# Kernel tuning notes

Hardware: AMD Instinct MI355X
Metric: run time of the kernel (lower is better)

The kernel has to match this reference:

```python
import jax, jax.numpy as jnp
import numpy as np

B, C, H, W = 8, 256, 64, 64
R = 8
CP = max(C // R, 3)  # C' = 32


def setup_inputs() -> dict:
    key = jax.random.key(0)
    ks = jax.random.split(key, 9)
    s_in = 1.0 / np.sqrt(C)
    s_cp = 1.0 / np.sqrt(CP)
    return {
        "x": jax.random.normal(ks[0], (B, C, H, W), dtype=jnp.float32),
        "Wq": jax.random.uniform(ks[1], (CP, C), minval=-s_in, maxval=s_in, dtype=jnp.float32),
        "bq": jax.random.uniform(ks[2], (CP,), minval=-s_in, maxval=s_in, dtype=jnp.float32),
        "Wk": jax.random.uniform(ks[3], (CP, C), minval=-s_in, maxval=s_in, dtype=jnp.float32),
        "bk": jax.random.uniform(ks[4], (CP,), minval=-s_in, maxval=s_in, dtype=jnp.float32),
        "Wv": jax.random.uniform(ks[5], (CP, C), minval=-s_in, maxval=s_in, dtype=jnp.float32),
        "bv": jax.random.uniform(ks[6], (CP,), minval=-s_in, maxval=s_in, dtype=jnp.float32),
        "Wb": jax.random.uniform(ks[7], (C, CP), minval=-s_cp, maxval=s_cp, dtype=jnp.float32),
        "bb": jax.random.uniform(ks[8], (C,), minval=-s_cp, maxval=s_cp, dtype=jnp.float32),
    }


def reference(x, Wq, bq, Wk, bk, Wv, bv, Wb, bb):
    b, c, h, w = x.shape
    n = h * w
    xf = x.reshape(b, c, n)  # [B, C, N]
    # 1x1 convs == channel-wise linear projections
    q = jnp.einsum('oc,bcn->bon', Wq, xf) + bq[None, :, None]  # [B, C', N]
    k = jnp.einsum('oc,bcn->bon', Wk, xf) + bk[None, :, None]
    v = jnp.einsum('oc,bcn->bon', Wv, xf) + bv[None, :, None]
    # attention: softmax(Q^T K) over last dim -> [B, N, N]
    attn = jax.nn.softmax(jnp.einsum('bon,bom->bnm', q, k), axis=-1)
    # out[b,c,i] = sum_j v[b,c,j] * attn[b,j,i]
    out = jnp.einsum('bcj,bji->bci', v, attn)  # [B, C', N]
    back = jnp.einsum('co,bon->bcn', Wb, out) + bb[None, :, None]  # [B, C, N]
    return back.reshape(b, c, h, w) + x
```

## Files before the change

kernel.cpp:

```cpp
#include <hip/hip_runtime.h>
#include <hip/hip_bf16.h>

#define NB 8
#define CC 256
#define CP 32
#define NN 4096
#define LOG2E 1.44269504088896340736f

typedef __attribute__((ext_vector_type(8))) short short8;
typedef __attribute__((ext_vector_type(4))) float floatx4;
typedef __attribute__((ext_vector_type(4))) int intx4;

static __device__ __forceinline__ ushort bf16r(float f) {
    __hip_bfloat16 h = __float2bfloat16(f);
    return *reinterpret_cast<ushort*>(&h);
}
static __device__ __forceinline__ float bf2f(ushort u) {
    union { unsigned int i; float f; } x;
    x.i = ((unsigned int)u) << 16;
    return x.f;
}
static __device__ __forceinline__ short8 load_frag(const ushort* p) {
    intx4 v = *reinterpret_cast<const intx4*>(p);
    return *reinterpret_cast<short8*>(&v);
}
static __device__ __forceinline__ unsigned int pk2(float a, float b) {
    unsigned int ua = __float_as_uint(a) + 0x8000u;
    unsigned int ub = __float_as_uint(b) + 0x8000u;
    return (ua >> 16) | (ub & 0xFFFF0000u);
}
static __device__ __forceinline__ ushort pk1(float a) {
    return (ushort)((__float_as_uint(a) + 0x8000u) >> 16);
}
static __device__ __forceinline__ float fexp2(float x) {
#if defined(__has_builtin)
#if __has_builtin(__builtin_amdgcn_exp2f)
    return __builtin_amdgcn_exp2f(x);
#else
    return __expf(x * 0.69314718055994530942f);
#endif
#else
    return __expf(x * 0.69314718055994530942f);
#endif
}

__global__ void prep_w(const float* __restrict__ Wq, const float* __restrict__ Wk,
                       const float* __restrict__ Wv, const float* __restrict__ Wb,
                       ushort* __restrict__ W96, ushort* __restrict__ W2b) {
    int r = blockIdx.x, c = threadIdx.x;
    if (r < 96) {
        const float* src = (r < 32) ? (Wq + r * CC) : ((r < 64) ? (Wk + (r - 32) * CC) : (Wv + (r - 64) * CC));
        float scale = (r < 32) ? LOG2E : 1.0f;
        W96[r * CC + c] = bf16r(src[c] * scale);
    } else {
        int idx = (r - 96) * 256 + c;
        W2b[idx] = bf16r(Wb[idx]);
    }
}

__global__ __launch_bounds__(256) void proj_kernel(
    const float* __restrict__ x, const ushort* __restrict__ W96,
    const float* __restrict__ bq, const float* __restrict__ bk, const float* __restrict__ bv,
    ushort* __restrict__ Qt, ushort* __restrict__ Kt, ushort* __restrict__ Vt) {
    __shared__ ushort xt[64 * 264];
    int b = blockIdx.x >> 6, nt = blockIdx.x & 63;
    int t = threadIdx.x;
    int n0 = nt * 64;
    {
        int cq = t >> 4, n4 = (t & 15) * 4;
#pragma unroll
        for (int cc = 0; cc < 4; cc++) {
            int c_base = cc * 64 + cq * 4;
            float4 xv[4];
#pragma unroll
            for (int e = 0; e < 4; e++)
                xv[e] = *reinterpret_cast<const float4*>(&x[((size_t)b * CC + c_base + e) * NN + n0 + n4]);
            const float* xs = reinterpret_cast<const float*>(xv);
#pragma unroll
            for (int jj = 0; jj < 4; jj++) {
                ushort4 u;
                u.x = pk1(xs[0 * 4 + jj]);
                u.y = pk1(xs[1 * 4 + jj]);
                u.z = pk1(xs[2 * 4 + jj]);
                u.w = pk1(xs[3 * 4 + jj]);
                *reinterpret_cast<ushort4*>(&xt[(n4 + jj) * 264 + c_base]) = u;
            }
        }
    }
    __syncthreads();
    int w = t >> 6, lane = t & 63, l15 = lane & 15, q = lane >> 4;
    floatx4 acc[6];
#pragma unroll
    for (int k = 0; k < 6; k++) acc[k] = (floatx4){0.f, 0.f, 0.f, 0.f};
#pragma unroll
    for (int ks = 0; ks < 8; ks++) {
        short8 bfrag = load_frag(&xt[(w * 16 + l15) * 264 + ks * 32 + q * 8]);
#pragma unroll
        for (int ot = 0; ot < 6; ot++) {
            short8 afrag = load_frag(&W96[(size_t)(ot * 16 + l15) * CC + ks * 32 + q * 8]);
            acc[ot] = __builtin_amdgcn_mfma_f32_16x16x32_bf16(afrag, bfrag, acc[ot], 0, 0, 0);
        }
    }
    int n = n0 + w * 16 + l15;
#pragma unroll
    for (int ot = 0; ot < 6; ot++) {
        const float* bias = (ot < 2) ? bq : ((ot < 4) ? bk : bv);
        ushort* dst = (ot < 2) ? Qt : ((ot < 4) ? Kt : Vt);
        int o0 = (ot & 1) * 16 + q * 4;
        float4 b4 = *reinterpret_cast<const float4*>(bias + o0);
        float sc = (ot < 2) ? LOG2E : 1.0f;
        ushort4 pk;
        pk.x = bf16r(acc[ot][0] + b4.x * sc);
        pk.y = bf16r(acc[ot][1] + b4.y * sc);
        pk.z = bf16r(acc[ot][2] + b4.z * sc);
        pk.w = bf16r(acc[ot][3] + b4.w * sc);
        *reinterpret_cast<ushort4*>(&dst[((size_t)b * NN + n) * CP + o0]) = pk;
    }
}

__global__ __launch_bounds__(256, 4) void passA_kernel(
    const ushort* __restrict__ Qt, const ushort* __restrict__ Kt, float* __restrict__ Fp) {
    __shared__ ushort kst[256 * 40];
    int bid = blockIdx.x;
    int mq = bid & 3, jt = (bid >> 2) & 63, b = bid >> 8;
    int w = threadIdx.x >> 6, lane = threadIdx.x & 63;
    int l15 = lane & 15, q = lane >> 4;
    int j = jt * 64 + w * 16 + l15;

    short8 af = load_frag(&Qt[((size_t)b * NN + j) * CP + q * 8]);
    floatx4 lacc = (floatx4){0.f, 0.f, 0.f, 0.f};

    for (int mc = 0; mc < 4; mc++) {
        int m0 = mq * 1024 + mc * 256;
        __syncthreads();
        {
            const intx4* src = reinterpret_cast<const intx4*>(&Kt[((size_t)b * NN + m0) * CP]);
            intx4* dst = reinterpret_cast<intx4*>(kst);
#pragma unroll
            for (int s = 0; s < 4; s++) {
                int g = threadIdx.x + 256 * s;
                dst[(g >> 2) * 5 + (g & 3)] = src[g];
            }
        }
        __syncthreads();
#pragma unroll
        for (int ms = 0; ms < 16; ms++) {
            short8 bf = load_frag(&kst[(ms * 16 + l15) * 40 + q * 8]);
            floatx4 z = (floatx4){0.f, 0.f, 0.f, 0.f};
            floatx4 s = __builtin_amdgcn_mfma_f32_16x16x32_bf16(af, bf, z, 0, 0, 0);
            lacc[0] += fexp2(s[0]);
            lacc[1] += fexp2(s[1]);
            lacc[2] += fexp2(s[2]);
            lacc[3] += fexp2(s[3]);
        }
    }
#pragma unroll
    for (int d = 1; d < 16; d <<= 1) {
        lacc[0] += __shfl_xor(lacc[0], d, 64);
        lacc[1] += __shfl_xor(lacc[1], d, 64);
        lacc[2] += __shfl_xor(lacc[2], d, 64);
        lacc[3] += __shfl_xor(lacc[3], d, 64);
    }
    if (l15 == 0) {
        float4 f4;
        f4.x = lacc[0]; f4.y = lacc[1]; f4.z = lacc[2]; f4.w = lacc[3];
        *reinterpret_cast<float4*>(&Fp[((size_t)mq * NB + b) * NN + jt * 64 + w * 16 + q * 4]) = f4;
    }
}

__global__ __launch_bounds__(256) void fold_kernel(
    const ushort* __restrict__ Vt, const float* __restrict__ Fp, ushort* __restrict__ Vp) {
    __shared__ ushort tile[32 * 136];
    const size_t PL = (size_t)NB * NN;
    int b = blockIdx.x >> 5, nc = blockIdx.x & 31;
    int t = threadIdx.x;
    int half = t >> 7, nl = t & 127;
    int n = nc * 128 + nl;
    size_t bn = (size_t)b * NN + n;
    float f = 1.0f / (Fp[bn] + Fp[PL + bn] + Fp[2 * PL + bn] + Fp[3 * PL + bn]);
    const ushort* src = &Vt[bn * CP + half * 16];
#pragma unroll
    for (int g = 0; g < 2; g++) {
        intx4 raw = *reinterpret_cast<const intx4*>(src + g * 8);
        const ushort* us = reinterpret_cast<const ushort*>(&raw);
#pragma unroll
        for (int e = 0; e < 8; e++) {
            tile[(half * 16 + g * 8 + e) * 136 + nl] = pk1(bf2f(us[e]) * f);
        }
    }
    __syncthreads();
#pragma unroll
    for (int cc = 0; cc < 16; cc++) {
        int c = half * 16 + cc;
        Vp[((size_t)b * CP + c) * NN + nc * 128 + nl] = tile[c * 136 + nl];
    }
}

__global__ __launch_bounds__(256, 4) void passB_kernel(
    const ushort* __restrict__ Qt, const ushort* __restrict__ Kt, const ushort* __restrict__ Vp,
    const ushort* __restrict__ W2b, const float* __restrict__ bb, const float* __restrict__ x,
    float* __restrict__ out) {
    __shared__ ushort qst[256 * 40];
    __shared__ ushort vst[32 * 264];

    int bid = blockIdx.x;
    int it = bid & 127, b = bid >> 7;
    int w = threadIdx.x >> 6, lane = threadIdx.x & 63;
    int l15 = lane & 15, q = lane >> 4;
    int jp = w;
    int i0 = it * 32;

    short8 kf0 = load_frag(&Kt[((size_t)b * NN + i0 + l15) * CP + q * 8]);
    short8 kf1 = load_frag(&Kt[((size_t)b * NN + i0 + 16 + l15) * CP + q * 8]);

    floatx4 acc00 = (floatx4){0.f, 0.f, 0.f, 0.f};
    floatx4 acc10 = (floatx4){0.f, 0.f, 0.f, 0.f};
    floatx4 acc01 = (floatx4){0.f, 0.f, 0.f, 0.f};
    floatx4 acc11 = (floatx4){0.f, 0.f, 0.f, 0.f};

    int qrow = (l15 >> 2) * 8 + (l15 & 3);

    for (int jc = 0; jc < 16; jc++) {
        int j0 = jc * 256;
        __syncthreads();
        {
            const intx4* qsrc = reinterpret_cast<const intx4*>(&Qt[((size_t)b * NN + j0) * CP]);
            intx4* qdst = reinterpret_cast<intx4*>(qst);
#pragma unroll
            for (int s = 0; s < 4; s++) {
                int g = threadIdx.x + 256 * s;
                qdst[(g >> 2) * 5 + (g & 3)] = qsrc[g];
            }
            int r = threadIdx.x >> 3, ci = threadIdx.x & 7;
            const intx4* vsrc = reinterpret_cast<const intx4*>(&Vp[((size_t)b * CP + r) * NN + j0]);
            intx4* vdst = reinterpret_cast<intx4*>(&vst[r * 264]);
#pragma unroll
            for (int s = 0; s < 4; s++) vdst[ci + 8 * s] = vsrc[ci + 8 * s];
        }
        __syncthreads();
#pragma unroll
        for (int ss = 0; ss < 2; ss++) {
            int jl = (ss * 4 + jp) * 32;
            short8 va0 = load_frag(&vst[l15 * 264 + jl + q * 8]);
            short8 va1 = load_frag(&vst[(16 + l15) * 264 + jl + q * 8]);
            short8 a0 = load_frag(&qst[(jl + qrow) * 40 + q * 8]);
            short8 a1 = load_frag(&qst[(jl + qrow + 4) * 40 + q * 8]);
            floatx4 z = (floatx4){0.f, 0.f, 0.f, 0.f};
            floatx4 s0A = __builtin_amdgcn_mfma_f32_16x16x32_bf16(a0, kf0, z, 0, 0, 0);
            floatx4 s1A = __builtin_amdgcn_mfma_f32_16x16x32_bf16(a1, kf0, z, 0, 0, 0);
            floatx4 s0B = __builtin_amdgcn_mfma_f32_16x16x32_bf16(a0, kf1, z, 0, 0, 0);
            floatx4 s1B = __builtin_amdgcn_mfma_f32_16x16x32_bf16(a1, kf1, z, 0, 0, 0);

            union { intx4 v; short8 s; } wa, wb2;
            wa.v.x = pk2(fexp2(s0A[0]), fexp2(s0A[1]));
            wa.v.y = pk2(fexp2(s0A[2]), fexp2(s0A[3]));
            wa.v.z = pk2(fexp2(s1A[0]), fexp2(s1A[1]));
            wa.v.w = pk2(fexp2(s1A[2]), fexp2(s1A[3]));
            wb2.v.x = pk2(fexp2(s0B[0]), fexp2(s0B[1]));
            wb2.v.y = pk2(fexp2(s0B[2]), fexp2(s0B[3]));
            wb2.v.z = pk2(fexp2(s1B[0]), fexp2(s1B[1]));
            wb2.v.w = pk2(fexp2(s1B[2]), fexp2(s1B[3]));

            acc00 = __builtin_amdgcn_mfma_f32_16x16x32_bf16(va0, wa.s, acc00, 0, 0, 0);
            acc10 = __builtin_amdgcn_mfma_f32_16x16x32_bf16(va1, wa.s, acc10, 0, 0, 0);
            acc01 = __builtin_amdgcn_mfma_f32_16x16x32_bf16(va0, wb2.s, acc01, 0, 0, 0);
            acc11 = __builtin_amdgcn_mfma_f32_16x16x32_bf16(va1, wb2.s, acc11, 0, 0, 0);
        }
    }

    __syncthreads();
    float* olds4 = reinterpret_cast<float*>(qst);
    int mbase = jp * (32 * 33);
#pragma unroll
    for (int r = 0; r < 4; r++) {
        olds4[mbase + (q * 4 + r) * 33 + l15] = acc00[r];
        olds4[mbase + (16 + q * 4 + r) * 33 + l15] = acc10[r];
        olds4[mbase + (q * 4 + r) * 33 + 16 + l15] = acc01[r];
        olds4[mbase + (16 + q * 4 + r) * 33 + 16 + l15] = acc11[r];
    }
    __syncthreads();

    short8 bfr[2];
#pragma unroll
    for (int s = 0; s < 2; s++) {
        float o8[8];
#pragma unroll
        for (int jj = 0; jj < 8; jj++) {
            int o = q * 8 + jj;
            int idx = o * 33 + s * 16 + l15;
            o8[jj] = olds4[idx] + olds4[1056 + idx] + olds4[2112 + idx] + olds4[3168 + idx];
        }
        union { intx4 v; short8 sh; } u;
        u.v.x = pk2(o8[0], o8[1]);
        u.v.y = pk2(o8[2], o8[3]);
        u.v.z = pk2(o8[4], o8[5]);
        u.v.w = pk2(o8[6], o8[7]);
        bfr[s] = u.sh;
    }
    int c0 = w * 64;
#pragma unroll
    for (int cs = 0; cs < 4; cs++) {
        short8 af = load_frag(&W2b[(size_t)(c0 + cs * 16 + l15) * CP + q * 8]);
#pragma unroll
        for (int s = 0; s < 2; s++) {
            floatx4 z = (floatx4){0.f, 0.f, 0.f, 0.f};
            floatx4 d = __builtin_amdgcn_mfma_f32_16x16x32_bf16(af, bfr[s], z, 0, 0, 0);
#pragma unroll
            for (int r = 0; r < 4; r++) {
                int c = c0 + cs * 16 + q * 4 + r;
                int i = i0 + s * 16 + l15;
                size_t idx = ((size_t)b * CC + c) * NN + i;
                out[idx] = d[r] + bb[c] + x[idx];
            }
        }
    }
}

extern "C" void kernel_launch(void* const* d_in, const int* in_sizes, int n_in,
                              void* d_out, int out_size, void* d_ws, size_t ws_size,
                              hipStream_t stream) {
    const float* x  = (const float*)d_in[0];
    const float* Wq = (const float*)d_in[1];
    const float* bq = (const float*)d_in[2];
    const float* Wk = (const float*)d_in[3];
    const float* bk = (const float*)d_in[4];
    const float* Wv = (const float*)d_in[5];
    const float* bv = (const float*)d_in[6];
    const float* Wb = (const float*)d_in[7];
    const float* bb = (const float*)d_in[8];
    float* out = (float*)d_out;

    char* ws = (char*)d_ws;
    ushort* Qt  = (ushort*)(ws);
    ushort* Kt  = (ushort*)(ws + (2u << 20));
    ushort* Vp  = (ushort*)(ws + (4u << 20));
    ushort* Vt  = (ushort*)(ws + (6u << 20));
    float*  Fp  = (float*) (ws + (8u << 20));
    ushort* W96 = (ushort*)(ws + (8u << 20) + (1u << 19));
    ushort* W2b = (ushort*)(ws + (8u << 20) + (1u << 19) + (48u << 10));

    prep_w<<<128, 256, 0, stream>>>(Wq, Wk, Wv, Wb, W96, W2b);
    proj_kernel<<<512, 256, 0, stream>>>(x, W96, bq, bk, bv, Qt, Kt, Vt);
    passA_kernel<<<2048, 256, 0, stream>>>(Qt, Kt, Fp);
    fold_kernel<<<256, 256, 0, stream>>>(Vt, Fp, Vp);
    passB_kernel<<<1024, 256, 0, stream>>>(Qt, Kt, Vp, W2b, bb, x, out);
}
```

Baseline: 164.7 us.

## Load Q/V fragments directly from global memory instead of staging through LDS

The passB kernel no longer cooperatively stages Q and V chunks into shared memory with two barriers per chunk. Each wave now loads its MFMA fragments straight from global memory (relying on L2/L1 caching) and walks an interleaved set of 32-column blocks. This shrinks LDS use, so the occupancy hint rises from 4 to 6 blocks per CU. The bf16 pack helper also uses a single byte-permute instruction. In exchange, every wave issues redundant, less coalesced global loads with no cross-wave reuse, and the kernel now depends on cache hits for latency hiding.

```diff
diff --git a/kernel.cpp b/kernel.cpp
--- a/kernel.cpp
+++ b/kernel.cpp
@@ -25,9 +25,13 @@
     return *reinterpret_cast<short8*>(&v);
 }
 static __device__ __forceinline__ unsigned int pk2(float a, float b) {
+#if defined(__has_builtin) && __has_builtin(__builtin_amdgcn_perm)
+    return __builtin_amdgcn_perm(__float_as_uint(b) + 0x8000u, __float_as_uint(a) + 0x8000u, 0x07060302u);
+#else
     unsigned int ua = __float_as_uint(a) + 0x8000u;
     unsigned int ub = __float_as_uint(b) + 0x8000u;
     return (ua >> 16) | (ub & 0xFFFF0000u);
+#endif
 }
 static __device__ __forceinline__ ushort pk1(float a) {
     return (ushort)((__float_as_uint(a) + 0x8000u) >> 16);
@@ -196,18 +200,16 @@
     }
 }
 
-__global__ __launch_bounds__(256, 4) void passB_kernel(
+__global__ __launch_bounds__(256, 6) void passB_kernel(
     const ushort* __restrict__ Qt, const ushort* __restrict__ Kt, const ushort* __restrict__ Vp,
     const ushort* __restrict__ W2b, const float* __restrict__ bb, const float* __restrict__ x,
     float* __restrict__ out) {
-    __shared__ ushort qst[256 * 40];
-    __shared__ ushort vst[32 * 264];
+    __shared__ float olds4[4 * 32 * 33];
 
     int bid = blockIdx.x;
     int it = bid & 127, b = bid >> 7;
     int w = threadIdx.x >> 6, lane = threadIdx.x & 63;
     int l15 = lane & 15, q = lane >> 4;
-    int jp = w;
     int i0 = it * 32;
 
     short8 kf0 = load_frag(&Kt[((size_t)b * NN + i0 + l15) * CP + q * 8]);
@@ -219,58 +221,41 @@
     floatx4 acc11 = (floatx4){0.f, 0.f, 0.f, 0.f};
 
     int qrow = (l15 >> 2) * 8 + (l15 & 3);
-
-    for (int jc = 0; jc < 16; jc++) {
-        int j0 = jc * 256;
-        __syncthreads();
-        {
-            const intx4* qsrc = reinterpret_cast<const intx4*>(&Qt[((size_t)b * NN + j0) * CP]);
-            intx4* qdst = reinterpret_cast<intx4*>(qst);
-#pragma unroll
-            for (int s = 0; s < 4; s++) {
-                int g = threadIdx.x + 256 * s;
-                qdst[(g >> 2) * 5 + (g & 3)] = qsrc[g];
-            }
-            int r = threadIdx.x >> 3, ci = threadIdx.x & 7;
-            const intx4* vsrc = reinterpret_cast<const intx4*>(&Vp[((size_t)b * CP + r) * NN + j0]);
-            intx4* vdst = reinterpret_cast<intx4*>(&vst[r * 264]);
-#pragma unroll
-            for (int s = 0; s < 4; s++) vdst[ci + 8 * s] = vsrc[ci + 8 * s];
-        }
-        __syncthreads();
-#pragma unroll
-        for (int ss = 0; ss < 2; ss++) {
-            int jl = (ss * 4 + jp) * 32;
-            short8 va0 = load_frag(&vst[l15 * 264 + jl + q * 8]);
-            short8 va1 = load_frag(&vst[(16 + l15) * 264 + jl + q * 8]);
-            short8 a0 = load_frag(&qst[(jl + qrow) * 40 + q * 8]);
-            short8 a1 = load_frag(&qst[(jl + qrow + 4) * 40 + q * 8]);
-            floatx4 z = (floatx4){0.f, 0.f, 0.f, 0.f};
-            floatx4 s0A = __builtin_amdgcn_mfma_f32_16x16x32_bf16(a0, kf0, z, 0, 0, 0);
-            floatx4 s1A = __builtin_amdgcn_mfma_f32_16x16x32_bf16(a1, kf0, z, 0, 0, 0);
-            floatx4 s0B = __builtin_amdgcn_mfma_f32_16x16x32_bf16(a0, kf1, z, 0, 0, 0);
-            floatx4 s1B = __builtin_amdgcn_mfma_f32_16x16x32_bf16(a1, kf1, z, 0, 0, 0);
-
-            union { intx4 v; short8 s; } wa, wb2;
-            wa.v.x = pk2(fexp2(s0A[0]), fexp2(s0A[1]));
-            wa.v.y = pk2(fexp2(s0A[2]), fexp2(s0A[3]));
-            wa.v.z = pk2(fexp2(s1A[0]), fexp2(s1A[1]));
-            wa.v.w = pk2(fexp2(s1A[2]), fexp2(s1A[3]));
-            wb2.v.x = pk2(fexp2(s0B[0]), fexp2(s0B[1]));
-            wb2.v.y = pk2(fexp2(s0B[2]), fexp2(s0B[3]));
-            wb2.v.z = pk2(fexp2(s1B[0]), fexp2(s1B[1]));
-            wb2.v.w = pk2(fexp2(s1B[2]), fexp2(s1B[3]));
-
-            acc00 = __builtin_amdgcn_mfma_f32_16x16x32_bf16(va0, wa.s, acc00, 0, 0, 0);
-            acc10 = __builtin_amdgcn_mfma_f32_16x16x32_bf16(va1, wa.s, acc10, 0, 0, 0);
-            acc01 = __builtin_amdgcn_mfma_f32_16x16x32_bf16(va0, wb2.s, acc01, 0, 0, 0);
-            acc11 = __builtin_amdgcn_mfma_f32_16x16x32_bf16(va1, wb2.s, acc11, 0, 0, 0);
-        }
-    }
-
-    __syncthreads();
-    float* olds4 = reinterpret_cast<float*>(qst);
-    int mbase = jp * (32 * 33);
+    const ushort* qbase = Qt + ((size_t)b * NN + qrow) * CP + q * 8;
+    const ushort* vbase0 = Vp + ((size_t)b * CP + l15) * NN + q * 8;
+    const ushort* vbase1 = Vp + ((size_t)b * CP + 16 + l15) * NN + q * 8;
+
+#pragma unroll 2
+    for (int jb = w; jb < 128; jb += 4) {
+        int j0 = jb * 32;
+        short8 a0 = load_frag(qbase + (size_t)j0 * CP);
+        short8 a1 = load_frag(qbase + (size_t)(j0 + 4) * CP);
+        short8 va0 = load_frag(vbase0 + j0);
+        short8 va1 = load_frag(vbase1 + j0);
+
+        floatx4 z = (floatx4){0.f, 0.f, 0.f, 0.f};
+        floatx4 s0A = __builtin_amdgcn_mfma_f32_16x16x32_bf16(a0, kf0, z, 0, 0, 0);
+        floatx4 s1A = __builtin_amdgcn_mfma_f32_16x16x32_bf16(a1, kf0, z, 0, 0, 0);
+        floatx4 s0B = __builtin_amdgcn_mfma_f32_16x16x32_bf16(a0, kf1, z, 0, 0, 0);
+        floatx4 s1B = __builtin_amdgcn_mfma_f32_16x16x32_bf16(a1, kf1, z, 0, 0, 0);
+
+        union { intx4 v; short8 s; } wa, wb2;
+        wa.v.x = pk2(fexp2(s0A[0]), fexp2(s0A[1]));
+        wa.v.y = pk2(fexp2(s0A[2]), fexp2(s0A[3]));
+        wa.v.z = pk2(fexp2(s1A[0]), fexp2(s1A[1]));
+        wa.v.w = pk2(fexp2(s1A[2]), fexp2(s1A[3]));
+        wb2.v.x = pk2(fexp2(s0B[0]), fexp2(s0B[1]));
+        wb2.v.y = pk2(fexp2(s0B[2]), fexp2(s0B[3]));
+        wb2.v.z = pk2(fexp2(s1B[0]), fexp2(s1B[1]));
+        wb2.v.w = pk2(fexp2(s1B[2]), fexp2(s1B[3]));
+
+        acc00 = __builtin_amdgcn_mfma_f32_16x16x32_bf16(va0, wa.s, acc00, 0, 0, 0);
+        acc10 = __builtin_amdgcn_mfma_f32_16x16x32_bf16(va1, wa.s, acc10, 0, 0, 0);
+        acc01 = __builtin_amdgcn_mfma_f32_16x16x32_bf16(va0, wb2.s, acc01, 0, 0, 0);
+        acc11 = __builtin_amdgcn_mfma_f32_16x16x32_bf16(va1, wb2.s, acc11, 0, 0, 0);
+    }
+
+    int mbase = w * (32 * 33);
 #pragma unroll
     for (int r = 0; r < 4; r++) {
         olds4[mbase + (q * 4 + r) * 33 + l15] = acc00[r];
```

New measurement: 182.1 us. 10.6% more time.
